# Performance work log

Measured on AMD Instinct MI355X. Metric: run time of the kernel, lower is better.

The kernel has to match this reference:

```python
import jax, jax.numpy as jnp
import numpy as np

N = 100000   # nodes
E = 1600000  # edges (avg degree 16)
IN, HID, OUT = 128, 128, 40
EPS = 1e-5   # BatchNorm1d default eps


def _lin(k, fan_in, fan_out):
    # Glorot-ish init for the linear weights
    return jax.random.normal(k, (fan_in, fan_out), jnp.float32) / np.sqrt(fan_in).astype(np.float32)


def setup_inputs() -> dict:
    key = jax.random.key(0)
    ks = jax.random.split(key, 12)
    return {
        "x": jax.random.normal(ks[0], (N, IN), jnp.float32),
        "edge_src": jax.random.randint(ks[1], (E,), 0, N, jnp.int32),
        "edge_dst": jax.random.randint(ks[2], (E,), 0, N, jnp.int32),
        # layer 0 (SAGEConv in->hid): lin_l (with bias) on aggregated neighbors, lin_r (no bias) on root
        "W_l0": _lin(ks[3], IN, HID), "b_l0": jnp.zeros((HID,), jnp.float32), "W_r0": _lin(ks[4], IN, HID),
        "g0": jnp.ones((HID,), jnp.float32), "be0": jnp.zeros((HID,), jnp.float32),
        # layer 1 (SAGEConv hid->hid)
        "W_l1": _lin(ks[5], HID, HID), "b_l1": jnp.zeros((HID,), jnp.float32), "W_r1": _lin(ks[6], HID, HID),
        "g1": jnp.ones((HID,), jnp.float32), "be1": jnp.zeros((HID,), jnp.float32),
        # layer 2 (SAGEConv hid->out)
        "W_l2": _lin(ks[7], HID, OUT), "b_l2": jnp.zeros((OUT,), jnp.float32), "W_r2": _lin(ks[8], HID, OUT),
    }


def reference(x, edge_src, edge_dst,
              W_l0, b_l0, W_r0, g0, be0,
              W_l1, b_l1, W_r1, g1, be1,
              W_l2, b_l2, W_r2):
    deg = jax.ops.segment_sum(jnp.ones((E,), x.dtype), edge_dst, num_segments=N)
    inv_deg = 1.0 / jnp.maximum(deg, 1.0)  # [N]

    def sage_conv(h, Wl, bl, Wr):
        # mean aggregation of neighbor features (gather + scatter-add), then two linears
        agg = jax.ops.segment_sum(h[edge_src], edge_dst, num_segments=N) * inv_deg[:, None]
        return agg @ Wl + bl + h @ Wr

    def bn(h, g, b):
        # BatchNorm1d in training mode: batch statistics over the node dimension
        m = h.mean(axis=0)
        v = h.var(axis=0)
        return (h - m) * (g / jnp.sqrt(v + EPS)) + b

    h = jax.nn.relu(bn(sage_conv(x, W_l0, b_l0, W_r0), g0, be0))
    h = jax.nn.relu(bn(sage_conv(h, W_l1, b_l1, W_r1), g1, be1))
    h = sage_conv(h, W_l2, b_l2, W_r2)
    return jax.nn.log_softmax(h, axis=-1)
```

## Files before the change

kernel.cpp:

```cpp
#include <hip/hip_runtime.h>
#include <hip/hip_bf16.h>

#define NNODES 100000
#define NEDGES 1600000
#define CH 128
#define OUTC 40
#define BN_EPS 1e-5f

typedef __attribute__((ext_vector_type(8))) short s8v;
typedef __attribute__((ext_vector_type(4))) float f32x4;

__device__ inline unsigned short f2bf_rn(float f) {
    unsigned u = __float_as_uint(f);
    return (unsigned short)((u + 0x7FFFu + ((u >> 16) & 1u)) >> 16);
}
__device__ inline float bf2f(unsigned short b) {
    return __uint_as_float((unsigned)b << 16);
}

__global__ void k_deg(const int* __restrict__ dst, int* __restrict__ deg) {
    int e = blockIdx.x * blockDim.x + threadIdx.x;
    if (e < NEDGES) atomicAdd(&deg[dst[e]], 1);
}

__global__ void k_scan1(const int* __restrict__ deg, int* __restrict__ row_ptr,
                        int* __restrict__ blkSums, float* __restrict__ inv_deg) {
    __shared__ int sd[256];
    int base = blockIdx.x * 1024 + threadIdx.x * 4;
    int t[4];
#pragma unroll
    for (int j = 0; j < 4; ++j) {
        int i = base + j;
        t[j] = (i < NNODES) ? deg[i] : 0;
        if (i < NNODES) inv_deg[i] = 1.0f / fmaxf((float)t[j], 1.0f);
    }
    int tsum = t[0] + t[1] + t[2] + t[3];
    sd[threadIdx.x] = tsum;
    __syncthreads();
    for (int off = 1; off < 256; off <<= 1) {
        int v = (threadIdx.x >= off) ? sd[threadIdx.x - off] : 0;
        __syncthreads();
        sd[threadIdx.x] += v;
        __syncthreads();
    }
    int run = sd[threadIdx.x] - tsum;
#pragma unroll
    for (int j = 0; j < 4; ++j) {
        int i = base + j;
        if (i < NNODES) row_ptr[i] = run;
        run += t[j];
    }
    if (threadIdx.x == 255) blkSums[blockIdx.x] = sd[255];
}

__global__ void k_scan2(int* blkSums, int nb) {
    if (threadIdx.x == 0 && blockIdx.x == 0) {
        int run = 0;
        for (int b = 0; b < nb; ++b) { int v = blkSums[b]; blkSums[b] = run; run += v; }
    }
}

__global__ void k_scan3(int* __restrict__ row_ptr, int* __restrict__ cursor,
                        const int* __restrict__ blkSums) {
    int i = blockIdx.x * blockDim.x + threadIdx.x;
    if (i < NNODES) {
        int v = row_ptr[i] + blkSums[i >> 10];
        row_ptr[i] = v;
        cursor[i] = v;
    }
    if (i == 0) row_ptr[NNODES] = NEDGES;
}

__global__ void k_fill(const int* __restrict__ src, const int* __restrict__ dst,
                       int* __restrict__ cursor, int* __restrict__ sorted_src) {
    int e = blockIdx.x * blockDim.x + threadIdx.x;
    if (e < NEDGES) {
        int d = dst[e];
        int pos = atomicAdd(&cursor[d], 1);
        sorted_src[pos] = src[e];
    }
}

__global__ void k_prepw(const float* __restrict__ Wl0, const float* __restrict__ Wr0,
                        const float* __restrict__ Wl1, const float* __restrict__ Wr1,
                        const float* __restrict__ Wl2, const float* __restrict__ Wr2,
                        short* __restrict__ wt) {
    int gid = blockIdx.x * 256 + threadIdx.x;
    const float* W;
    int col, k, base, halfsz;
    float val;
    if (gid < 65536) {
        int w = gid >> 14;
        int r = gid & 16383;
        col = r >> 7; k = r & 127;
        W = (w == 0) ? Wl0 : (w == 1) ? Wr0 : (w == 2) ? Wl1 : Wr1;
        val = W[k * 128 + col];
        base = w * 32768; halfsz = 16384;
    } else if (gid < 77824) {
        int r2 = gid - 65536;
        int w = r2 / 6144;
        int r = r2 - w * 6144;
        col = r >> 7; k = r & 127;
        W = w ? Wr2 : Wl2;
        val = (col < OUTC) ? W[k * OUTC + col] : 0.f;
        base = 131072 + w * 12288; halfsz = 6144;
    } else {
        return;
    }
    unsigned short hi = f2bf_rn(val);
    unsigned short lo = f2bf_rn(val - bf2f(hi));
    int idx = col * 128 + k;
    wt[base + idx] = (short)hi;
    wt[base + halfsz + idx] = (short)lo;
}

template <int WRW, int WCW, int RF, int CF, int WCOLS, int NCR, int LSZ, bool BN_A>
__global__ __launch_bounds__(256, 1) void k_gemm_mfma(
    const float* __restrict__ H,
    const short* __restrict__ WtL, const short* __restrict__ WtR,
    const float* __restrict__ bias,
    const float* __restrict__ bnscale, const float* __restrict__ bnshift,
    float* __restrict__ yl, float* __restrict__ yr) {
    __shared__ short A_hi[128 * 128];
    __shared__ short A_lo[128 * 128];
    __shared__ short B_hi[WCOLS * 128];
    __shared__ short B_lo[WCOLS * 128];

    int tid = threadIdx.x;
    int row0 = blockIdx.x * 128;

#pragma unroll
    for (int i = 0; i < 8; ++i) {
        int c = tid + 256 * i;
        int r = c >> 4;
        int k0 = (c & 15) << 3;
        int gr = row0 + r;
        float f[8];
        if (gr < NNODES) {
            float4 v0 = *(const float4*)&H[(size_t)gr * CH + k0];
            float4 v1 = *(const float4*)&H[(size_t)gr * CH + k0 + 4];
            f[0] = v0.x; f[1] = v0.y; f[2] = v0.z; f[3] = v0.w;
            f[4] = v1.x; f[5] = v1.y; f[6] = v1.z; f[7] = v1.w;
        } else {
#pragma unroll
            for (int j = 0; j < 8; ++j) f[j] = 0.f;
        }
        if (BN_A) {
            float4 s0 = *(const float4*)&bnscale[k0];
            float4 s1 = *(const float4*)&bnscale[k0 + 4];
            float4 h0 = *(const float4*)&bnshift[k0];
            float4 h1 = *(const float4*)&bnshift[k0 + 4];
            f[0] = fmaxf(fmaf(f[0], s0.x, h0.x), 0.f);
            f[1] = fmaxf(fmaf(f[1], s0.y, h0.y), 0.f);
            f[2] = fmaxf(fmaf(f[2], s0.z, h0.z), 0.f);
            f[3] = fmaxf(fmaf(f[3], s0.w, h0.w), 0.f);
            f[4] = fmaxf(fmaf(f[4], s1.x, h1.x), 0.f);
            f[5] = fmaxf(fmaf(f[5], s1.y, h1.y), 0.f);
            f[6] = fmaxf(fmaf(f[6], s1.z, h1.z), 0.f);
            f[7] = fmaxf(fmaf(f[7], s1.w, h1.w), 0.f);
        }
        s8v hi8, lo8;
#pragma unroll
        for (int j = 0; j < 8; ++j) {
            unsigned short h = f2bf_rn(f[j]);
            hi8[j] = (short)h;
            lo8[j] = (short)f2bf_rn(f[j] - bf2f(h));
        }
        int e = ((r << 7) + k0) ^ ((r & 7) << 3);
        *(s8v*)&A_hi[e] = hi8;
        *(s8v*)&A_lo[e] = lo8;
    }

    int lane = tid & 63;
    int wid = tid >> 6;
    int wr = wid / WCW, wc = wid % WCW;
    int l15 = lane & 15, kb = lane >> 4;
    int rowbase = wr * RF * 16;
    int colbase = wc * CF * 16;

    for (int half = 0; half < 2; ++half) {
        if (half == 1) __syncthreads();
        const short* Wt = half ? WtR : WtL;
        constexpr int WCHUNK = WCOLS * 16;
#pragma unroll
        for (int i = 0; i < (WCHUNK + 255) / 256; ++i) {
            int c = tid + 256 * i;
            if (c < WCHUNK) {
                int col = c >> 4;
                int k0 = (c & 15) << 3;
                s8v hi8 = *(const s8v*)&Wt[col * 128 + k0];
                s8v lo8 = *(const s8v*)&Wt[LSZ + col * 128 + k0];
                int e = ((col << 7) + k0) ^ ((col & 7) << 3);
                *(s8v*)&B_hi[e] = hi8;
                *(s8v*)&B_lo[e] = lo8;
            }
        }
        __syncthreads();

        f32x4 acc[RF][CF];
#pragma unroll
        for (int i = 0; i < RF; ++i)
#pragma unroll
            for (int j = 0; j < CF; ++j) acc[i][j] = (f32x4){0.f, 0.f, 0.f, 0.f};

#pragma unroll
        for (int ks = 0; ks < 4; ++ks) {
            s8v ah[RF], al[RF];
#pragma unroll
            for (int rf = 0; rf < RF; ++rf) {
                int r = rowbase + rf * 16 + l15;
                int e = ((r << 7) + ks * 32 + (kb << 3)) ^ ((r & 7) << 3);
                ah[rf] = *(const s8v*)&A_hi[e];
                al[rf] = *(const s8v*)&A_lo[e];
            }
#pragma unroll
            for (int cf = 0; cf < CF; ++cf) {
                int cc = colbase + cf * 16 + l15;
                int e = ((cc << 7) + ks * 32 + (kb << 3)) ^ ((cc & 7) << 3);
                s8v bh = *(const s8v*)&B_hi[e];
                s8v bl = *(const s8v*)&B_lo[e];
#pragma unroll
                for (int rf = 0; rf < RF; ++rf) {
                    acc[rf][cf] = __builtin_amdgcn_mfma_f32_16x16x32_bf16(ah[rf], bh, acc[rf][cf], 0, 0, 0);
                    acc[rf][cf] = __builtin_amdgcn_mfma_f32_16x16x32_bf16(al[rf], bh, acc[rf][cf], 0, 0, 0);
                    acc[rf][cf] = __builtin_amdgcn_mfma_f32_16x16x32_bf16(ah[rf], bl, acc[rf][cf], 0, 0, 0);
                }
            }
        }

        float* Y = half ? yr : yl;
#pragma unroll
        for (int cf = 0; cf < CF; ++cf) {
            int gcol = colbase + cf * 16 + l15;
            float bb = 0.f;
            if (half == 1 && gcol < NCR) bb = bias[gcol];
#pragma unroll
            for (int rf = 0; rf < RF; ++rf) {
#pragma unroll
                for (int r = 0; r < 4; ++r) {
                    int grow = row0 + rowbase + rf * 16 + (lane >> 4) * 4 + r;
                    if (grow < NNODES && gcol < NCR)
                        Y[(size_t)grow * NCR + gcol] = acc[rf][cf][r] + bb;
                }
            }
        }
    }
}

__global__ void k_combine128(const float* __restrict__ yl, const int* __restrict__ row_ptr,
                             const int* __restrict__ sorted_src, const float* __restrict__ inv_deg,
                             float* __restrict__ z) {
    int wave = threadIdx.x >> 6, lane = threadIdx.x & 63;
    int node = blockIdx.x * 4 + wave;
    if (node >= NNODES) return;
    int s0 = row_ptr[node], s1 = row_ptr[node + 1];
    const float2* Y = (const float2*)yl;
    float ax0 = 0.f, ay0 = 0.f, ax1 = 0.f, ay1 = 0.f;
    float ax2 = 0.f, ay2 = 0.f, ax3 = 0.f, ay3 = 0.f;
    int e = s0;
    for (; e + 4 <= s1; e += 4) {
        int i0 = sorted_src[e], i1 = sorted_src[e + 1];
        int i2 = sorted_src[e + 2], i3 = sorted_src[e + 3];
        float2 v0 = Y[(size_t)i0 * 64 + lane];
        float2 v1 = Y[(size_t)i1 * 64 + lane];
        float2 v2 = Y[(size_t)i2 * 64 + lane];
        float2 v3 = Y[(size_t)i3 * 64 + lane];
        ax0 += v0.x; ay0 += v0.y; ax1 += v1.x; ay1 += v1.y;
        ax2 += v2.x; ay2 += v2.y; ax3 += v3.x; ay3 += v3.y;
    }
    for (; e < s1; ++e) {
        int i = sorted_src[e];
        float2 v = Y[(size_t)i * 64 + lane];
        ax0 += v.x; ay0 += v.y;
    }
    float w = inv_deg[node];
    float2* Z = (float2*)z;
    float2 r = Z[(size_t)node * 64 + lane];
    r.x += (ax0 + ax1 + ax2 + ax3) * w;
    r.y += (ay0 + ay1 + ay2 + ay3) * w;
    Z[(size_t)node * 64 + lane] = r;
}

__global__ void k_combine40_lsm(const float* __restrict__ yl, const float* __restrict__ yr,
                                const int* __restrict__ row_ptr, const int* __restrict__ sorted_src,
                                const float* __restrict__ inv_deg, float* __restrict__ out) {
    int wave = threadIdx.x >> 6, lane = threadIdx.x & 63;
    int node = blockIdx.x * 4 + wave;
    if (node >= NNODES) return;
    bool act = lane < 20;
    int s0 = row_ptr[node], s1 = row_ptr[node + 1];
    float ax0 = 0.f, ay0 = 0.f, ax1 = 0.f, ay1 = 0.f;
    float ax2 = 0.f, ay2 = 0.f, ax3 = 0.f, ay3 = 0.f;
    int e = s0;
    for (; e + 4 <= s1; e += 4) {
        int i0 = sorted_src[e], i1 = sorted_src[e + 1];
        int i2 = sorted_src[e + 2], i3 = sorted_src[e + 3];
        if (act) {
            float2 v0 = *(const float2*)&yl[(size_t)i0 * OUTC + lane * 2];
            float2 v1 = *(const float2*)&yl[(size_t)i1 * OUTC + lane * 2];
            float2 v2 = *(const float2*)&yl[(size_t)i2 * OUTC + lane * 2];
            float2 v3 = *(const float2*)&yl[(size_t)i3 * OUTC + lane * 2];
            ax0 += v0.x; ay0 += v0.y; ax1 += v1.x; ay1 += v1.y;
            ax2 += v2.x; ay2 += v2.y; ax3 += v3.x; ay3 += v3.y;
        }
    }
    for (; e < s1; ++e) {
        int i = sorted_src[e];
        if (act) {
            float2 v = *(const float2*)&yl[(size_t)i * OUTC + lane * 2];
            ax0 += v.x; ay0 += v.y;
        }
    }
    float zx = 0.f, zy = 0.f;
    if (act) {
        float w = inv_deg[node];
        float2 r = *(const float2*)&yr[(size_t)node * OUTC + lane * 2];
        zx = (ax0 + ax1 + ax2 + ax3) * w + r.x;
        zy = (ay0 + ay1 + ay2 + ay3) * w + r.y;
    }
    float m = act ? fmaxf(zx, zy) : -INFINITY;
#pragma unroll
    for (int off = 1; off <= 16; off <<= 1) m = fmaxf(m, __shfl_xor(m, off));
    float se = act ? (expf(zx - m) + expf(zy - m)) : 0.f;
#pragma unroll
    for (int off = 1; off <= 16; off <<= 1) se += __shfl_xor(se, off);
    float lse = m + logf(se);
    if (act) {
        float2 o = make_float2(zx - lse, zy - lse);
        *(float2*)&out[(size_t)node * OUTC + lane * 2] = o;
    }
}

__global__ void k_stats(const float* __restrict__ h, float* __restrict__ sums) {
    __shared__ float ls[256], ls2[256];
    int c = threadIdx.x & 127;
    int half = threadIdx.x >> 7;
    float s = 0.f, s2 = 0.f;
    for (int r = blockIdx.x * 2 + half; r < NNODES; r += gridDim.x * 2) {
        float v = h[(size_t)r * CH + c];
        s += v; s2 += v * v;
    }
    ls[threadIdx.x] = s; ls2[threadIdx.x] = s2;
    __syncthreads();
    if (half == 0) {
        atomicAdd(&sums[c], ls[c] + ls[c + 128]);
        atomicAdd(&sums[CH + c], ls2[c] + ls2[c + 128]);
    }
}

__global__ void k_bn_finalize(const float* __restrict__ sums, const float* __restrict__ g,
                              const float* __restrict__ be, float* __restrict__ scale,
                              float* __restrict__ shift) {
    int c = threadIdx.x;
    if (c < CH) {
        float mean = sums[c] * (1.0f / NNODES);
        float var = sums[128 + c] * (1.0f / NNODES) - mean * mean;
        float sc = g[c] * rsqrtf(var + BN_EPS);
        scale[c] = sc;
        shift[c] = be[c] - mean * sc;
    }
}

extern "C" void kernel_launch(void* const* d_in, const int* in_sizes, int n_in,
                              void* d_out, int out_size, void* d_ws, size_t ws_size,
                              hipStream_t stream) {
    const float* x   = (const float*)d_in[0];
    const int* esrc  = (const int*)d_in[1];
    const int* edst  = (const int*)d_in[2];
    const float* W_l0 = (const float*)d_in[3];
    const float* b_l0 = (const float*)d_in[4];
    const float* W_r0 = (const float*)d_in[5];
    const float* g0   = (const float*)d_in[6];
    const float* be0  = (const float*)d_in[7];
    const float* W_l1 = (const float*)d_in[8];
    const float* b_l1 = (const float*)d_in[9];
    const float* W_r1 = (const float*)d_in[10];
    const float* g1   = (const float*)d_in[11];
    const float* be1  = (const float*)d_in[12];
    const float* W_l2 = (const float*)d_in[13];
    const float* b_l2 = (const float*)d_in[14];
    const float* W_r2 = (const float*)d_in[15];
    float* out = (float*)d_out;

    char* w = (char*)d_ws;
    size_t o = 0;
    auto nxt = [&](size_t b) { void* p = w + o; o = (o + b + 511) & ~(size_t)511; return p; };
    int* deg      = (int*)nxt((size_t)NNODES * 4);
    int* row_ptr  = (int*)nxt((size_t)(NNODES + 1) * 4);
    int* cursor   = (int*)nxt((size_t)NNODES * 4);
    float* invdeg = (float*)nxt((size_t)NNODES * 4);
    int* blkSums  = (int*)nxt(128 * 4);
    float* sums   = (float*)nxt(512 * 4);
    float* scsh   = (float*)nxt(512 * 4);
    short* wtbuf  = (short*)nxt(155648 * 2);
    int* sorted   = (int*)nxt((size_t)NEDGES * 4);
    float* ylbuf  = (float*)nxt((size_t)NNODES * CH * 4);
    float* zA     = (float*)nxt((size_t)NNODES * CH * 4);
    float* zB     = (float*)nxt((size_t)NNODES * CH * 4);
    float* sums0 = sums, *sums1 = sums + 256;
    float* scale0 = scsh, *shift0 = scsh + 128, *scale1 = scsh + 256, *shift1 = scsh + 384;

    const short* wtL0 = wtbuf;
    const short* wtR0 = wtbuf + 32768;
    const short* wtL1 = wtbuf + 65536;
    const short* wtR1 = wtbuf + 98304;
    const short* wtL2 = wtbuf + 131072;
    const short* wtR2 = wtbuf + 143360;

    hipMemsetAsync(deg, 0, (size_t)NNODES * 4, stream);
    hipMemsetAsync(sums, 0, 512 * 4, stream);

    const int EB = (NEDGES + 255) / 256;
    const int SCAN_B = (NNODES + 1023) / 1024;
    const int NB = (NNODES + 255) / 256;
    const int COMB_B = (NNODES + 3) / 4;
    const int GEMM_B = (NNODES + 127) / 128;

    k_prepw<<<304, 256, 0, stream>>>(W_l0, W_r0, W_l1, W_r1, W_l2, W_r2, wtbuf);
    k_deg<<<EB, 256, 0, stream>>>(edst, deg);
    k_scan1<<<SCAN_B, 256, 0, stream>>>(deg, row_ptr, blkSums, invdeg);
    k_scan2<<<1, 64, 0, stream>>>(blkSums, SCAN_B);
    k_scan3<<<NB, 256, 0, stream>>>(row_ptr, cursor, blkSums);
    k_fill<<<EB, 256, 0, stream>>>(esrc, edst, cursor, sorted);

    k_gemm_mfma<2, 2, 4, 4, 128, 128, 16384, false><<<GEMM_B, 256, 0, stream>>>(
        x, wtL0, wtR0, b_l0, nullptr, nullptr, ylbuf, zA);
    k_combine128<<<COMB_B, 256, 0, stream>>>(ylbuf, row_ptr, sorted, invdeg, zA);
    k_stats<<<256, 256, 0, stream>>>(zA, sums0);
    k_bn_finalize<<<1, 128, 0, stream>>>(sums0, g0, be0, scale0, shift0);

    k_gemm_mfma<2, 2, 4, 4, 128, 128, 16384, true><<<GEMM_B, 256, 0, stream>>>(
        zA, wtL1, wtR1, b_l1, scale0, shift0, ylbuf, zB);
    k_combine128<<<COMB_B, 256, 0, stream>>>(ylbuf, row_ptr, sorted, invdeg, zB);
    k_stats<<<256, 256, 0, stream>>>(zB, sums1);
    k_bn_finalize<<<1, 128, 0, stream>>>(sums1, g1, be1, scale1, shift1);

    k_gemm_mfma<4, 1, 2, 3, 48, 40, 6144, true><<<GEMM_B, 256, 0, stream>>>(
        zB, wtL2, wtR2, b_l2, scale1, shift1, ylbuf, zA);
    k_combine40_lsm<<<COMB_B, 256, 0, stream>>>(ylbuf, zA, row_ptr, sorted, invdeg, out);
}
```

Measured before the change: 1.010 ms.

## Replace per-node CSR fill with bucketed edge sort and LDS-atomic aggregation

Replaces the per-edge global-atomic CSR fill with a bucket sort into 128-node buckets. Each block counts its edges per bucket in shared memory, claims a range per bucket with one global atomic, then writes (src,dst) pairs. The combine kernels now give each 128-node bucket to one block, accumulate neighbour features with shared-memory float atomics in a 64KB LDS tile, and then apply inv_deg and the root term. The single-thread block-sum scan is also parallelised. This cuts global atomic contention in the fill and balances work across waves, but it adds many LDS atomics, doubles edge storage to int2, and the large LDS footprint limits occupancy.

Result: slower. 3.842 ms (+280.5%).

```diff
diff --git a/kernel.cpp b/kernel.cpp
--- a/kernel.cpp
+++ b/kernel.cpp
@@ -6,6 +6,9 @@
 #define CH 128
 #define OUTC 40
 #define BN_EPS 1e-5f
+#define NBUCK 782
+#define FILL_BLOCKS 128
+#define EPB (NEDGES / FILL_BLOCKS)
 
 typedef __attribute__((ext_vector_type(8))) short s8v;
 typedef __attribute__((ext_vector_type(4))) float f32x4;
@@ -53,31 +56,53 @@
     if (threadIdx.x == 255) blkSums[blockIdx.x] = sd[255];
 }
 
-__global__ void k_scan2(int* blkSums, int nb) {
-    if (threadIdx.x == 0 && blockIdx.x == 0) {
-        int run = 0;
-        for (int b = 0; b < nb; ++b) { int v = blkSums[b]; blkSums[b] = run; run += v; }
-    }
-}
-
-__global__ void k_scan3(int* __restrict__ row_ptr, int* __restrict__ cursor,
-                        const int* __restrict__ blkSums) {
+__global__ void k_scan2(int* __restrict__ blkSums, int nb) {
+    __shared__ int sd[128];
+    int t = threadIdx.x;
+    int v = (t < nb) ? blkSums[t] : 0;
+    sd[t] = v;
+    __syncthreads();
+    for (int off = 1; off < 128; off <<= 1) {
+        int u = (t >= off) ? sd[t - off] : 0;
+        __syncthreads();
+        sd[t] += u;
+        __syncthreads();
+    }
+    if (t < nb) blkSums[t] = sd[t] - v;
+}
+
+__global__ void k_scan3(int* __restrict__ row_ptr, const int* __restrict__ blkSums) {
     int i = blockIdx.x * blockDim.x + threadIdx.x;
-    if (i < NNODES) {
-        int v = row_ptr[i] + blkSums[i >> 10];
-        row_ptr[i] = v;
-        cursor[i] = v;
-    }
+    if (i < NNODES) row_ptr[i] += blkSums[i >> 10];
     if (i == 0) row_ptr[NNODES] = NEDGES;
 }
 
-__global__ void k_fill(const int* __restrict__ src, const int* __restrict__ dst,
-                       int* __restrict__ cursor, int* __restrict__ sorted_src) {
-    int e = blockIdx.x * blockDim.x + threadIdx.x;
-    if (e < NEDGES) {
+__global__ void k_binit(const int* __restrict__ row_ptr, int* __restrict__ bcur) {
+    int b = blockIdx.x * 256 + threadIdx.x;
+    if (b < NBUCK) bcur[b] = row_ptr[b << 7];
+}
+
+__global__ __launch_bounds__(256) void k_fillb(const int* __restrict__ src,
+                                               const int* __restrict__ dst,
+                                               int* __restrict__ bcur,
+                                               int2* __restrict__ tmp) {
+    __shared__ int h[NBUCK];
+    int tid = threadIdx.x;
+    int e0 = blockIdx.x * EPB;
+    for (int i = tid; i < NBUCK; i += 256) h[i] = 0;
+    __syncthreads();
+    for (int e = e0 + tid; e < e0 + EPB; e += 256)
+        atomicAdd(&h[dst[e] >> 7], 1);
+    __syncthreads();
+    for (int b = tid; b < NBUCK; b += 256) {
+        int c = h[b];
+        h[b] = c ? atomicAdd(&bcur[b], c) : 0;
+    }
+    __syncthreads();
+    for (int e = e0 + tid; e < e0 + EPB; e += 256) {
         int d = dst[e];
-        int pos = atomicAdd(&cursor[d], 1);
-        sorted_src[pos] = src[e];
+        int pos = atomicAdd(&h[d >> 7], 1);
+        tmp[pos] = make_int2(src[e], d);
     }
 }
 
@@ -247,87 +272,108 @@
     }
 }
 
-__global__ void k_combine128(const float* __restrict__ yl, const int* __restrict__ row_ptr,
-                             const int* __restrict__ sorted_src, const float* __restrict__ inv_deg,
-                             float* __restrict__ z) {
-    int wave = threadIdx.x >> 6, lane = threadIdx.x & 63;
-    int node = blockIdx.x * 4 + wave;
-    if (node >= NNODES) return;
-    int s0 = row_ptr[node], s1 = row_ptr[node + 1];
-    const float2* Y = (const float2*)yl;
-    float ax0 = 0.f, ay0 = 0.f, ax1 = 0.f, ay1 = 0.f;
-    float ax2 = 0.f, ay2 = 0.f, ax3 = 0.f, ay3 = 0.f;
-    int e = s0;
-    for (; e + 4 <= s1; e += 4) {
-        int i0 = sorted_src[e], i1 = sorted_src[e + 1];
-        int i2 = sorted_src[e + 2], i3 = sorted_src[e + 3];
-        float2 v0 = Y[(size_t)i0 * 64 + lane];
-        float2 v1 = Y[(size_t)i1 * 64 + lane];
-        float2 v2 = Y[(size_t)i2 * 64 + lane];
-        float2 v3 = Y[(size_t)i3 * 64 + lane];
-        ax0 += v0.x; ay0 += v0.y; ax1 += v1.x; ay1 += v1.y;
-        ax2 += v2.x; ay2 += v2.y; ax3 += v3.x; ay3 += v3.y;
-    }
-    for (; e < s1; ++e) {
-        int i = sorted_src[e];
-        float2 v = Y[(size_t)i * 64 + lane];
-        ax0 += v.x; ay0 += v.y;
-    }
-    float w = inv_deg[node];
-    float2* Z = (float2*)z;
-    float2 r = Z[(size_t)node * 64 + lane];
-    r.x += (ax0 + ax1 + ax2 + ax3) * w;
-    r.y += (ay0 + ay1 + ay2 + ay3) * w;
-    Z[(size_t)node * 64 + lane] = r;
-}
-
-__global__ void k_combine40_lsm(const float* __restrict__ yl, const float* __restrict__ yr,
-                                const int* __restrict__ row_ptr, const int* __restrict__ sorted_src,
-                                const float* __restrict__ inv_deg, float* __restrict__ out) {
-    int wave = threadIdx.x >> 6, lane = threadIdx.x & 63;
-    int node = blockIdx.x * 4 + wave;
-    if (node >= NNODES) return;
+__global__ __launch_bounds__(256) void k_combineb128(
+    const float* __restrict__ yl, const int2* __restrict__ tmp,
+    const int* __restrict__ row_ptr, const float* __restrict__ inv_deg,
+    float* __restrict__ z) {
+    __shared__ float acc[128 * 128];
+    int tid = threadIdx.x;
+    int node0 = blockIdx.x << 7;
+    for (int i = tid; i < 128 * 32; i += 256)
+        ((float4*)acc)[i] = make_float4(0.f, 0.f, 0.f, 0.f);
+    int s0 = row_ptr[node0];
+    int s1 = row_ptr[min(node0 + 128, NNODES)];
+    __syncthreads();
+    int lane = tid & 63, wid = tid >> 6;
+    int cnt = s1 - s0;
+    int es = s0 + (int)(((long)cnt * wid) >> 2);
+    int ee = s0 + (int)(((long)cnt * (wid + 1)) >> 2);
+    int e = es;
+    for (; e + 4 <= ee; e += 4) {
+        int2 d0 = tmp[e], d1 = tmp[e + 1], d2 = tmp[e + 2], d3 = tmp[e + 3];
+        float vx0 = yl[(size_t)d0.x * 128 + lane];
+        float vy0 = yl[(size_t)d0.x * 128 + 64 + lane];
+        float vx1 = yl[(size_t)d1.x * 128 + lane];
+        float vy1 = yl[(size_t)d1.x * 128 + 64 + lane];
+        float vx2 = yl[(size_t)d2.x * 128 + lane];
+        float vy2 = yl[(size_t)d2.x * 128 + 64 + lane];
+        float vx3 = yl[(size_t)d3.x * 128 + lane];
+        float vy3 = yl[(size_t)d3.x * 128 + 64 + lane];
+        atomicAdd(&acc[((d0.y & 127) << 7) + lane], vx0);
+        atomicAdd(&acc[((d0.y & 127) << 7) + 64 + lane], vy0);
+        atomicAdd(&acc[((d1.y & 127) << 7) + lane], vx1);
+        atomicAdd(&acc[((d1.y & 127) << 7) + 64 + lane], vy1);
+        atomicAdd(&acc[((d2.y & 127) << 7) + lane], vx2);
+        atomicAdd(&acc[((d2.y & 127) << 7) + 64 + lane], vy2);
+        atomicAdd(&acc[((d3.y & 127) << 7) + lane], vx3);
+        atomicAdd(&acc[((d3.y & 127) << 7) + 64 + lane], vy3);
+    }
+    for (; e < ee; ++e) {
+        int2 d = tmp[e];
+        float vx = yl[(size_t)d.x * 128 + lane];
+        float vy = yl[(size_t)d.x * 128 + 64 + lane];
+        atomicAdd(&acc[((d.y & 127) << 7) + lane], vx);
+        atomicAdd(&acc[((d.y & 127) << 7) + 64 + lane], vy);
+    }
+    __syncthreads();
+    int nn = min(128, NNODES - node0);
+    for (int i = tid; i < nn * 32; i += 256) {
+        int row = i >> 5, c4 = (i & 31) << 2;
+        float4 a = *(float4*)&acc[(row << 7) + c4];
+        float w = inv_deg[node0 + row];
+        float4 zr = *(float4*)&z[(((size_t)(node0 + row)) << 7) + c4];
+        zr.x += a.x * w; zr.y += a.y * w; zr.z += a.z * w; zr.w += a.w * w;
+        *(float4*)&z[(((size_t)(node0 + row)) << 7) + c4] = zr;
+    }
+}
+
+__global__ __launch_bounds__(256) void k_combineb40(
+    const float* __restrict__ yl, const int2* __restrict__ tmp,
+    const int* __restrict__ row_ptr, const float* __restrict__ inv_deg,
+    const float* __restrict__ yr, float* __restrict__ out) {
+    __shared__ float acc[128 * 40];
+    int tid = threadIdx.x;
+    int node0 = blockIdx.x << 7;
+    for (int i = tid; i < 128 * 10; i += 256)
+        ((float4*)acc)[i] = make_float4(0.f, 0.f, 0.f, 0.f);
+    int s0 = row_ptr[node0];
+    int s1 = row_ptr[min(node0 + 128, NNODES)];
+    __syncthreads();
+    int lane = tid & 63, wid = tid >> 6;
     bool act = lane < 20;
-    int s0 = row_ptr[node], s1 = row_ptr[node + 1];
-    float ax0 = 0.f, ay0 = 0.f, ax1 = 0.f, ay1 = 0.f;
-    float ax2 = 0.f, ay2 = 0.f, ax3 = 0.f, ay3 = 0.f;
-    int e = s0;
-    for (; e + 4 <= s1; e += 4) {
-        int i0 = sorted_src[e], i1 = sorted_src[e + 1];
-        int i2 = sorted_src[e + 2], i3 = sorted_src[e + 3];
+    int cnt = s1 - s0;
+    int es = s0 + (int)(((long)cnt * wid) >> 2);
+    int ee = s0 + (int)(((long)cnt * (wid + 1)) >> 2);
+    for (int e = es; e < ee; ++e) {
+        int2 d = tmp[e];
         if (act) {
-            float2 v0 = *(const float2*)&yl[(size_t)i0 * OUTC + lane * 2];
-            float2 v1 = *(const float2*)&yl[(size_t)i1 * OUTC + lane * 2];
-            float2 v2 = *(const float2*)&yl[(size_t)i2 * OUTC + lane * 2];
-            float2 v3 = *(const float2*)&yl[(size_t)i3 * OUTC + lane * 2];
-            ax0 += v0.x; ay0 += v0.y; ax1 += v1.x; ay1 += v1.y;
-            ax2 += v2.x; ay2 += v2.y; ax3 += v3.x; ay3 += v3.y;
-        }
-    }
-    for (; e < s1; ++e) {
-        int i = sorted_src[e];
+            float2 v = *(const float2*)&yl[(size_t)d.x * OUTC + lane * 2];
+            atomicAdd(&acc[(d.y & 127) * OUTC + lane * 2], v.x);
+            atomicAdd(&acc[(d.y & 127) * OUTC + lane * 2 + 1], v.y);
+        }
+    }
+    __syncthreads();
+    for (int i = wid; i < 128; i += 4) {
+        int node = node0 + i;
+        if (node >= NNODES) break;
+        float zx = 0.f, zy = 0.f;
         if (act) {
-            float2 v = *(const float2*)&yl[(size_t)i * OUTC + lane * 2];
-            ax0 += v.x; ay0 += v.y;
-        }
-    }
-    float zx = 0.f, zy = 0.f;
-    if (act) {
-        float w = inv_deg[node];
-        float2 r = *(const float2*)&yr[(size_t)node * OUTC + lane * 2];
-        zx = (ax0 + ax1 + ax2 + ax3) * w + r.x;
-        zy = (ay0 + ay1 + ay2 + ay3) * w + r.y;
-    }
-    float m = act ? fmaxf(zx, zy) : -INFINITY;
-#pragma unroll
-    for (int off = 1; off <= 16; off <<= 1) m = fmaxf(m, __shfl_xor(m, off));
-    float se = act ? (expf(zx - m) + expf(zy - m)) : 0.f;
-#pragma unroll
-    for (int off = 1; off <= 16; off <<= 1) se += __shfl_xor(se, off);
-    float lse = m + logf(se);
-    if (act) {
-        float2 o = make_float2(zx - lse, zy - lse);
-        *(float2*)&out[(size_t)node * OUTC + lane * 2] = o;
+            float w = inv_deg[node];
+            float2 r = *(const float2*)&yr[(size_t)node * OUTC + lane * 2];
+            zx = acc[i * OUTC + lane * 2] * w + r.x;
+            zy = acc[i * OUTC + lane * 2 + 1] * w + r.y;
+        }
+        float m = act ? fmaxf(zx, zy) : -INFINITY;
+#pragma unroll
+        for (int off = 1; off <= 16; off <<= 1) m = fmaxf(m, __shfl_xor(m, off));
+        float se = act ? (expf(zx - m) + expf(zy - m)) : 0.f;
+#pragma unroll
+        for (int off = 1; off <= 16; off <<= 1) se += __shfl_xor(se, off);
+        float lse = m + logf(se);
+        if (act) {
+            float2 o = make_float2(zx - lse, zy - lse);
+            *(float2*)&out[(size_t)node * OUTC + lane * 2] = o;
+        }
     }
 }
 
@@ -387,13 +433,13 @@
     auto nxt = [&](size_t b) { void* p = w + o; o = (o + b + 511) & ~(size_t)511; return p; };
     int* deg      = (int*)nxt((size_t)NNODES * 4);
     int* row_ptr  = (int*)nxt((size_t)(NNODES + 1) * 4);
-    int* cursor   = (int*)nxt((size_t)NNODES * 4);
     float* invdeg = (float*)nxt((size_t)NNODES * 4);
     int* blkSums  = (int*)nxt(128 * 4);
+    int* bcur     = (int*)nxt(NBUCK * 4);
     float* sums   = (float*)nxt(512 * 4);
     float* scsh   = (float*)nxt(512 * 4);
     short* wtbuf  = (short*)nxt(155648 * 2);
-    int* sorted   = (int*)nxt((size_t)NEDGES * 4);
+    int2* tmp     = (int2*)nxt((size_t)NEDGES * 8);
     float* ylbuf  = (float*)nxt((size_t)NNODES * CH * 4);
     float* zA     = (float*)nxt((size_t)NNODES * CH * 4);
     float* zB     = (float*)nxt((size_t)NNODES * CH * 4);
@@ -413,29 +459,29 @@
     const int EB = (NEDGES + 255) / 256;
     const int SCAN_B = (NNODES + 1023) / 1024;
     const int NB = (NNODES + 255) / 256;
-    const int COMB_B = (NNODES + 3) / 4;
     const int GEMM_B = (NNODES + 127) / 128;
 
     k_prepw<<<304, 256, 0, stream>>>(W_l0, W_r0, W_l1, W_r1, W_l2, W_r2, wtbuf);
     k_deg<<<EB, 256, 0, stream>>>(edst, deg);
     k_scan1<<<SCAN_B, 256, 0, stream>>>(deg, row_ptr, blkSums, invdeg);
-    k_scan2<<<1, 64, 0, stream>>>(blkSums, SCAN_B);
-    k_scan3<<<NB, 256, 0, stream>>>(row_ptr, cursor, blkSums);
-    k_fill<<<EB, 256, 0, stream>>>(esrc, edst, cursor, sorted);
+    k_scan2<<<1, 128, 0, stream>>>(blkSums, SCAN_B);
+    k_scan3<<<NB, 256, 0, stream>>>(row_ptr, blkSums);
+    k_binit<<<4, 256, 0, stream>>>(row_ptr, bcur);
+    k_fillb<<<FILL_BLOCKS, 256, 0, stream>>>(esrc, edst, bcur, tmp);
 
     k_gemm_mfma<2, 2, 4, 4, 128, 128, 16384, false><<<GEMM_B, 256, 0, stream>>>(
         x, wtL0, wtR0, b_l0, nullptr, nullptr, ylbuf, zA);
-    k_combine128<<<COMB_B, 256, 0, stream>>>(ylbuf, row_ptr, sorted, invdeg, zA);
+    k_combineb128<<<NBUCK, 256, 0, stream>>>(ylbuf, tmp, row_ptr, invdeg, zA);
     k_stats<<<256, 256, 0, stream>>>(zA, sums0);
     k_bn_finalize<<<1, 128, 0, stream>>>(sums0, g0, be0, scale0, shift0);
 
     k_gemm_mfma<2, 2, 4, 4, 128, 128, 16384, true><<<GEMM_B, 256, 0, stream>>>(
         zA, wtL1, wtR1, b_l1, scale0, shift0, ylbuf, zB);
-    k_combine128<<<COMB_B, 256, 0, stream>>>(ylbuf, row_ptr, sorted, invdeg, zB);
+    k_combineb128<<<NBUCK, 256, 0, stream>>>(ylbuf, tmp, row_ptr, invdeg, zB);
     k_stats<<<256, 256, 0, stream>>>(zB, sums1);
     k_bn_finalize<<<1, 128, 0, stream>>>(sums1, g1, be1, scale1, shift1);
 
     k_gemm_mfma<4, 1, 2, 3, 48, 40, 6144, true><<<GEMM_B, 256, 0, stream>>>(
         zB, wtL2, wtR2, b_l2, scale1, shift1, ylbuf, zA);
-    k_combine40_lsm<<<COMB_B, 256, 0, stream>>>(ylbuf, zA, row_ptr, sorted, invdeg, out);
-}
+    k_combineb40<<<NBUCK, 256, 0, stream>>>(ylbuf, tmp, row_ptr, invdeg, zA, out);
+}
```
